# Kernel tuning notes

Hardware: AMD Instinct MI355X
Metric: run time of the kernel (lower is better)

## Reference

```python
import jax, jax.numpy as jnp
import numpy as np

LN_EPS = 1e-5

def _layer_norm(x, w, b):
    mu = jnp.mean(x, axis=-1, keepdims=True)
    var = jnp.mean(jnp.square(x - mu), axis=-1, keepdims=True)
    return (x - mu) * jax.lax.rsqrt(var + LN_EPS) * w + b

def setup_inputs() -> dict:
    key = jax.random.key(0)
    ks = jax.random.split(key, 8)
    B, NODES, D = 32, 202, 64
    return {
        "embeddings": jax.random.normal(ks[0], (B, NODES, D), dtype=jnp.float32),
        "ln_w": jnp.ones((D,), jnp.float32),
        "ln_b": jnp.zeros((D,), jnp.float32),
        "W1_w": jax.random.normal(ks[1], (D, D), jnp.float32) * 0.05,
        "W1_b": jax.random.normal(ks[2], (D,), jnp.float32) * 0.05,
        "W2_w": jax.random.normal(ks[3], (D, D), jnp.float32) * 0.05,
        "W2_b": jax.random.normal(ks[4], (D,), jnp.float32) * 0.05,
        "a1_w": jax.random.normal(ks[5], (3 * D,), jnp.float32) * 0.05,
        "a1_b": jax.random.normal(ks[6], (1,), jnp.float32) * 0.05,
        "a2_w": jax.random.normal(ks[7], (3 * D,), jnp.float32) * 0.05,
        "a2_b": jax.random.normal(jax.random.fold_in(key, 99), (1,), jnp.float32) * 0.05,
    }

def reference(embeddings, ln_w, ln_b, W1_w, W1_b, W2_w, W2_b, a1_w, a1_b, a2_w, a2_b):
    # embeddings: [B, 2+N, D]; dropout p=0 (eval) -> identity
    emb = _layer_norm(embeddings, ln_w, ln_b)
    uid0 = emb[:, 0, :]          # [B, D]
    iid0 = emb[:, 1, :]          # [B, D]
    iatt = emb[:, 2:, :]         # [B, N, D]
    ua = uid0[:, None, :] * iatt  # [B, N, D]
    # value[b,i,j,:] = LN(ua[b,i] * ua[b,j])  -- the big [B,N,N,D] tensor
    value = _layer_norm(ua[:, :, None, :] * ua[:, None, :, :], ln_w, ln_b)

    def head(Ww, Wb, aw, ab):
        # Linear W applied to expanded query/key/iid collapses to per-row projections;
        # a([wq; wk; wiid]) decomposes additively across the three concat blocks.
        wua = ua @ Ww.T + Wb                  # [B, N, D]  (shared by query rows and key cols)
        wiid = iid0 @ Ww.T + Wb               # [B, D]
        aq, ak, ai = jnp.split(aw, 3)
        sq = wua @ aq                         # [B, N]  query contribution (index i)
        sk = wua @ ak                         # [B, N]  key contribution (index j)
        si = wiid @ ai                        # [B]
        scores = sq[:, :, None] + sk[:, None, :] + si[:, None, None] + ab[0]  # [B,N,N]
        scores = jax.nn.leaky_relu(scores)    # negative_slope=0.01 (torch default)
        alphas = jax.nn.softmax(scores, axis=-1)
        # original sums over dim=-2 (index i), softmax was over j -- kept faithfully
        return jnp.einsum('bij,bijd->bjd', alphas, value)  # [B, N, D]

    att1 = head(W1_w, W1_b, a1_w, a1_b)
    att2 = head(W2_w, W2_b, a2_w, a2_b)
    att_value = (att1 + att2) * 0.5           # [B, N, D]
    ui = (uid0 * iid0)[:, None, :]            # [B, 1, D]
    em_out = jnp.concatenate([ui, att_value], axis=1)  # [B, N+1, D]
    return jax.nn.leaky_relu(em_out)
```

## Files before the change

kernel.cpp:

```cpp
#include <hip/hip_runtime.h>
#include <hip/hip_bf16.h>

#define LN_EPS 1e-5f
#define BB 32
#define NI 200
#define DD 64

typedef __attribute__((ext_vector_type(8))) short bf16x8;
typedef __attribute__((ext_vector_type(4))) short bf16x4;
typedef __attribute__((ext_vector_type(4))) float f32x4;

__device__ __forceinline__ float leaky(float x) { return fmaxf(x, 0.01f * x); }
__device__ __forceinline__ short f2bf(float x) {
  __hip_bfloat16 h = __float2bfloat16(x);
  return *reinterpret_cast<short*>(&h);
}
__device__ __forceinline__ float bf2fs(short s) {
  unsigned u = ((unsigned)(unsigned short)s) << 16;
  return __uint_as_float(u);
}

__device__ __forceinline__ void reduce2(float& a, float& b) {
#pragma unroll
  for (int m = 1; m < 64; m <<= 1) { a += __shfl_xor(a, m, 64); b += __shfl_xor(b, m, 64); }
}
__device__ __forceinline__ void reduce3(float& a, float& b, float& c) {
#pragma unroll
  for (int m = 1; m < 64; m <<= 1) {
    a += __shfl_xor(a, m, 64); b += __shfl_xor(b, m, 64); c += __shfl_xor(c, m, 64);
  }
}
__device__ __forceinline__ void rmax2(float& a, float& b) {
#pragma unroll
  for (int m = 1; m < 64; m <<= 1) {
    a = fmaxf(a, __shfl_xor(a, m, 64));
    b = fmaxf(b, __shfl_xor(b, m, 64));
  }
}

#define SM_G    0
#define SM_UA   52544
#define SM_UA2  79168
#define SM_UAT  105792
#define SM_ST   134464
#define SM_KV   139456
#define SM_V    141120
#define SM_PART 142656
#define SM_WMX  143680
#define SM_MISC 143744
#define SM_LN   143776
#define SM_TOTAL 145408

__global__ void __launch_bounds__(512, 1)
gat_fused(const float* __restrict__ emb,
          const float* __restrict__ lw,
          const float* __restrict__ lb,
          const float* __restrict__ W1,
          const float* __restrict__ W1b,
          const float* __restrict__ W2,
          const float* __restrict__ W2b,
          const float* __restrict__ a1,
          const float* __restrict__ a1b,
          const float* __restrict__ a2,
          const float* __restrict__ a2b,
          float* __restrict__ out) {
  __shared__ __align__(16) char smem[SM_TOTAL];
  float* sY   = (float*)(smem + SM_G);
  short* sUA  = (short*)(smem + SM_UA);
  short* sUA2 = (short*)(smem + SM_UA2);
  short* sUAT = (short*)(smem + SM_UAT);
  float* sST  = (float*)(smem + SM_ST);
  float* sKV  = (float*)(smem + SM_KV);
  float* sV   = (float*)(smem + SM_V);
  float* sPart = (float*)(smem + SM_PART);
  float* wmx  = (float*)(smem + SM_WMX);
  float* sMisc = (float*)(smem + SM_MISC);
  float* sLN  = (float*)(smem + SM_LN);

  int b = blockIdx.y, bx = blockIdx.x, tid = threadIdx.x;
  int wv = tid >> 6, lane = tid & 63, q = lane >> 4, col = lane & 15;

  for (int idx = tid; idx < 202 * 16; idx += 512) {
    int r = idx >> 4, qd = (idx & 15) << 2;
    f32x4 v = *(const f32x4*)(emb + ((size_t)b * 202 + r) * 64 + qd);
    float* dst = sY + r * 65 + qd;
    dst[0] = v.x; dst[1] = v.y; dst[2] = v.z; dst[3] = v.w;
  }
  if (wv == 0) {
    float p0 = 0, p1 = 0;
#pragma unroll 8
    for (int d = 0; d < 64; d++) {
      float x = W1[d * 64 + lane];
      p0 = fmaf(x, a1[d], p0); p1 = fmaf(x, a1[64 + d], p1);
    }
    sV[0 * 64 + lane] = p0; sV[1 * 64 + lane] = p1;
  } else if (wv == 1) {
    float p0 = 0, p1 = 0;
#pragma unroll 8
    for (int d = 0; d < 64; d++) {
      float x = W2[d * 64 + lane];
      p0 = fmaf(x, a2[d], p0); p1 = fmaf(x, a2[64 + d], p1);
    }
    sV[2 * 64 + lane] = p0; sV[3 * 64 + lane] = p1;
  } else if (wv == 2) {
    float p = 0;
#pragma unroll 8
    for (int d = 0; d < 64; d++) p = fmaf(W1[d * 64 + lane], a1[128 + d], p);
    sV[4 * 64 + lane] = p;
    float c0 = W1b[lane] * a1[lane];
    float c1 = W1b[lane] * a1[64 + lane];
    float c2 = W1b[lane] * a1[128 + lane];
    reduce3(c0, c1, c2);
    if (lane == 0) { sMisc[0] = c0; sMisc[1] = c1; sMisc[2] = c2; }
  } else if (wv == 3) {
    float p = 0;
#pragma unroll 8
    for (int d = 0; d < 64; d++) p = fmaf(W2[d * 64 + lane], a2[128 + d], p);
    sV[5 * 64 + lane] = p;
    float c3 = W2b[lane] * a2[lane];
    float c4 = W2b[lane] * a2[64 + lane];
    float c5 = W2b[lane] * a2[128 + lane];
    reduce3(c3, c4, c5);
    if (lane == 0) { sMisc[3] = c3; sMisc[4] = c4; sMisc[5] = c5; }
  }
  __syncthreads();

  {
    int o = tid & 7, rr = tid >> 3;
#pragma unroll
    for (int r0 = 0; r0 < 256; r0 += 64) {
      int r = r0 + rr;
      float s = 0.f, s2 = 0.f;
      if (r < 202) {
        const float* xr = sY + r * 65 + o * 8;
#pragma unroll
        for (int k = 0; k < 8; k++) { float x = xr[k]; s += x; s2 = fmaf(x, x, s2); }
      }
#pragma unroll
      for (int m = 1; m < 8; m <<= 1) {
        s += __shfl_xor(s, m, 64); s2 += __shfl_xor(s2, m, 64);
      }
      if (r < 202 && o == 0) {
        float mu = s * (1.f / 64);
        float var = fmaxf(s2 * (1.f / 64) - mu * mu, 0.f);
        sLN[r * 2] = mu;
        sLN[r * 2 + 1] = rsqrtf(var + LN_EPS);
      }
    }
  }
  __syncthreads();

  {
    int d = tid & 63;
    float w = lw[d], bi = lb[d];
    for (int idx = tid; idx < 202 * 64; idx += 512) {
      int r = idx >> 6;
      float mu = sLN[r * 2], rinv = sLN[r * 2 + 1];
      float x = sY[r * 65 + d];
      sY[r * 65 + d] = (x - mu) * rinv * w + bi;
    }
  }
  __syncthreads();

  if (wv == 0) {
    float u0 = sY[lane];
    float iid = sY[65 + lane];
    out[(size_t)(b * 201) * 64 + lane] = leaky(u0 * iid);
    float q0 = iid * sV[4 * 64 + lane], q1 = iid * sV[5 * 64 + lane];
    reduce2(q0, q1);
    if (lane == 0) {
      sMisc[6] = q0 + sMisc[2] + a1b[0];
      sMisc[7] = q1 + sMisc[5] + a2b[0];
    }
  }
  for (int idx = tid; idx < 1664; idx += 512) {
    int itile = idx >> 7, rem = idx & 127, kh = rem >> 6, ln = rem & 63;
    int node = itile * 16 + (ln & 15);
    int dbase = kh * 32 + (ln >> 4) * 8;
    bf16x8 pk, pk2;
    if (node < NI) {
      const float* yr = sY + (2 + node) * 65 + dbase;
#pragma unroll
      for (int k = 0; k < 8; k++) {
        float v = sY[dbase + k] * yr[k];
        short h = f2bf(v);
        pk[k] = h;
        float f = bf2fs(h);
        pk2[k] = f2bf(f * f);
      }
    } else {
#pragma unroll
      for (int k = 0; k < 8; k++) { pk[k] = 0; pk2[k] = 0; }
    }
    *(bf16x8*)(sUA + idx * 8) = pk;
    *(bf16x8*)(sUA2 + idx * 8) = pk2;
  }
  {
    int d = tid & 63, ir = (tid >> 6) & 3, ph = tid >> 8;
    float ud = sY[d];
    for (int p = ph; p < 7; p += 2) {
      int i0 = p * 32 + ir * 8;
      bf16x8 pk;
#pragma unroll
      for (int uu = 0; uu < 8; uu++) {
        int node = i0 + uu;
        pk[uu] = (node < NI) ? f2bf(ud * sY[(2 + node) * 65 + d]) : (short)0;
      }
      int off = ((p * 4 + (d >> 4)) * 64 + ((d & 15) + 16 * ir)) * 8;
      *(bf16x8*)(sUAT + off) = pk;
    }
  }
  {
    int o = tid & 7, rr = tid >> 3;
    float uv0[8], uv1[8], uv2[8], uv3[8];
#pragma unroll
    for (int k = 0; k < 8; k++) {
      float u0k = sY[o * 8 + k];
      uv0[k] = u0k * sV[0 * 64 + o * 8 + k];
      uv1[k] = u0k * sV[1 * 64 + o * 8 + k];
      uv2[k] = u0k * sV[2 * 64 + o * 8 + k];
      uv3[k] = u0k * sV[3 * 64 + o * 8 + k];
    }
#pragma unroll
    for (int r0 = 0; r0 < 256; r0 += 64) {
      int i = r0 + rr;
      float p0 = 0, p1 = 0, p2 = 0, p3 = 0;
      if (i < NI) {
        const float* yr = sY + (2 + i) * 65 + o * 8;
#pragma unroll
        for (int k = 0; k < 8; k++) {
          float y = yr[k];
          p0 = fmaf(y, uv0[k], p0); p1 = fmaf(y, uv1[k], p1);
          p2 = fmaf(y, uv2[k], p2); p3 = fmaf(y, uv3[k], p3);
        }
      }
#pragma unroll
      for (int m = 1; m < 8; m <<= 1) {
        p0 += __shfl_xor(p0, m, 64); p1 += __shfl_xor(p1, m, 64);
        p2 += __shfl_xor(p2, m, 64); p3 += __shfl_xor(p3, m, 64);
      }
      if (i < NI && o == 0) {
        sST[i * 6 + 0] = p0 + sMisc[0];
        sST[i * 6 + 3] = p2 + sMisc[3];
        sKV[0 * 208 + i] = p1 + sMisc[1];
        sKV[1 * 208 + i] = p3 + sMisc[4];
      }
    }
  }
  if (tid < 48) sST[1200 + tid] = 0.f;
  if (tid < 16) sKV[(tid >> 3) * 208 + 200 + (tid & 7)] = 0.f;
  __syncthreads();

  {
    float m1 = (tid < NI) ? sKV[tid] : -3e38f;
    float m2 = (tid < NI) ? sKV[208 + tid] : -3e38f;
    rmax2(m1, m2);
    if (lane == 0) { wmx[wv * 2] = m1; wmx[wv * 2 + 1] = m2; }
  }
  __syncthreads();

  {
    int sh = -1, si = 0;
    if (tid < NI) { sh = 0; si = tid; }
    else if (tid >= 256 && tid < 256 + NI) { sh = 1; si = tid - 256; }
    if (sh >= 0) {
      float mx = -3e38f;
#pragma unroll
      for (int k = 0; k < 8; k++) mx = fmaxf(mx, wmx[k * 2 + sh]);
      float* st = sST + si * 6;
      float base = st[sh * 3] + sMisc[6 + sh];
      st[sh * 3] = base;
      float rm = leaky(base + mx);
      const float* skh = sKV + sh * 208;
      float d0 = 0, d1 = 0, d2 = 0, d3 = 0;
      for (int j = 0; j < NI; j += 4) {
        float s0 = base + skh[j + 0]; d0 += __expf(fmaxf(s0, 0.01f * s0) - rm);
        float s1 = base + skh[j + 1]; d1 += __expf(fmaxf(s1, 0.01f * s1) - rm);
        float s2 = base + skh[j + 2]; d2 += __expf(fmaxf(s2, 0.01f * s2) - rm);
        float s3 = base + skh[j + 3]; d3 += __expf(fmaxf(s3, 0.01f * s3) - rm);
      }
      st[sh * 3 + 1] = rm;
      st[sh * 3 + 2] = 1.0f / ((d0 + d1) + (d2 + d3));
    }
  }
  __syncthreads();

  int half = wv >> 2, wq = wv & 3;
  int jt = bx * 2 + half;
  bool act = (jt < 13);
  short* sG0 = (short*)(smem + SM_G);
  short* sG1 = (short*)(smem + SM_G + 7168);
  short* sGh = half ? sG1 : sG0;
  float* sPh = sPart + half * 128;

  if (tid < 128) ((int*)sG0)[1664 + tid] = 0;
  else if (tid < 256) ((int*)sG1)[1664 + (tid - 128)] = 0;

  if (act) {
    bf16x8 bf0 = *(bf16x8*)(sUA + ((jt * 2 + 0) * 64 + lane) * 8);
    bf16x8 bf1 = *(bf16x8*)(sUA + ((jt * 2 + 1) * 64 + lane) * 8);
    bf16x8 b2f0 = *(bf16x8*)(sUA2 + ((jt * 2 + 0) * 64 + lane) * 8);
    bf16x8 b2f1 = *(bf16x8*)(sUA2 + ((jt * 2 + 1) * 64 + lane) * 8);
    int jglob = jt * 16 + col;
    float skj1 = sKV[jglob], skj2 = sKV[208 + jglob];
    float mpart = 0.f, spart = 0.f;
    for (int it = wq; it < 13; it += 4) {
      bf16x8 af0 = *(bf16x8*)(sUA + ((it * 2 + 0) * 64 + lane) * 8);
      bf16x8 af1 = *(bf16x8*)(sUA + ((it * 2 + 1) * 64 + lane) * 8);
      bf16x8 a2f0 = *(bf16x8*)(sUA2 + ((it * 2 + 0) * 64 + lane) * 8);
      bf16x8 a2f1 = *(bf16x8*)(sUA2 + ((it * 2 + 1) * 64 + lane) * 8);
      f32x4 s = {0, 0, 0, 0}, t = {0, 0, 0, 0};
      s = __builtin_amdgcn_mfma_f32_16x16x32_bf16(af0, bf0, s, 0, 0, 0);
      s = __builtin_amdgcn_mfma_f32_16x16x32_bf16(af1, bf1, s, 0, 0, 0);
      t = __builtin_amdgcn_mfma_f32_16x16x32_bf16(a2f0, b2f0, t, 0, 0, 0);
      t = __builtin_amdgcn_mfma_f32_16x16x32_bf16(a2f1, b2f1, t, 0, 0, 0);
      bf16x4 gp;
#pragma unroll
      for (int r = 0; r < 4; r++) {
        int i = it * 16 + q * 4 + r;
        const float* st = sST + i * 6;
        float mu = s[r] * (1.f / 64);
        float var = fmaxf(t[r] * (1.f / 64) - mu * mu, 0.f);
        float inv = rsqrtf(var + LN_EPS);
        float sc1 = st[0] + skj1;
        float e1 = __expf(fmaxf(sc1, 0.01f * sc1) - st[1]) * st[2];
        float sc2 = st[3] + skj2;
        float e2 = __expf(fmaxf(sc2, 0.01f * sc2) - st[4]) * st[5];
        float c = 0.5f * (e1 + e2);
        float g = c * inv;
        mpart = fmaf(g, mu, mpart);
        spart += c;
        gp[r] = f2bf(g);
      }
      int kl = (it & 1) * 16 + q * 4;
      int off = ((it >> 1) * 64 + (col + 16 * (kl >> 3))) * 8 + (kl & 7);
      *(bf16x4*)(sGh + off) = gp;
    }
    mpart += __shfl_xor(mpart, 16, 64); mpart += __shfl_xor(mpart, 32, 64);
    spart += __shfl_xor(spart, 16, 64); spart += __shfl_xor(spart, 32, 64);
    if (lane < 16) {
      sPh[(wq * 2 + 0) * 16 + lane] = mpart;
      sPh[(wq * 2 + 1) * 16 + lane] = spart;
    }
  }
  __syncthreads();

  if (act) {
    f32x4 acc = {0, 0, 0, 0};
#pragma unroll
    for (int kt = 0; kt < 7; kt++) {
      bf16x8 ga = *(bf16x8*)(sGh + (kt * 64 + lane) * 8);
      bf16x8 ub = *(bf16x8*)(sUAT + ((kt * 4 + wq) * 64 + lane) * 8);
      acc = __builtin_amdgcn_mfma_f32_16x16x32_bf16(ga, ub, acc, 0, 0, 0);
    }
    int d = wq * 16 + col;
    float w = lw[d], bia = lb[d];
#pragma unroll
    for (int r = 0; r < 4; r++) {
      int jl = q * 4 + r, jg = jt * 16 + jl;
      if (jg < NI) {
        float m = sPh[0 * 16 + jl] + sPh[2 * 16 + jl] +
                  sPh[4 * 16 + jl] + sPh[6 * 16 + jl];
        float S = sPh[1 * 16 + jl] + sPh[3 * 16 + jl] +
                  sPh[5 * 16 + jl] + sPh[7 * 16 + jl];
        int cn = jt * 128 + (d >> 5) * 64 + ((d >> 3) & 3) * 16 + (jg & 15);
        float uajd = bf2fs(sUA[cn * 8 + (d & 7)]);
        float att = w * (uajd * acc[r] - m) + bia * S;
        out[(size_t)(b * 201 + 1 + jg) * 64 + d] = leaky(att);
      }
    }
  }
}

extern "C" void kernel_launch(void* const* d_in, const int* in_sizes, int n_in,
                              void* d_out, int out_size, void* d_ws, size_t ws_size,
                              hipStream_t stream) {
  const float* emb = (const float*)d_in[0];
  const float* lw  = (const float*)d_in[1];
  const float* lb  = (const float*)d_in[2];
  const float* W1  = (const float*)d_in[3];
  const float* W1b = (const float*)d_in[4];
  const float* W2  = (const float*)d_in[5];
  const float* W2b = (const float*)d_in[6];
  const float* a1  = (const float*)d_in[7];
  const float* a1b = (const float*)d_in[8];
  const float* a2  = (const float*)d_in[9];
  const float* a2b = (const float*)d_in[10];
  float* out = (float*)d_out;

  gat_fused<<<dim3(7, BB), dim3(512), 0, stream>>>(emb, lw, lb, W1, W1b, W2, W2b,
                                                   a1, a1b, a2, a2b, out);
}
```

Baseline: 94.48 us.

## Split fused kernel into three stages to deduplicate per-batch preprocessing

Before this change, each of the 7 blocks per batch redundantly recomputed LayerNorm, the bf16 ua/ua² tiles, the transposed tiles, the projections and the softmax statistics. Now a first kernel spreads that preprocessing over 13 node tiles per batch and writes it to workspace. A second kernel computes the row max and softmax denominators, and the main kernel only copies the staged data from global memory into shared memory. This removes redundant work and adds parallelism to the prologue, at the cost of two extra launches and a global-memory round trip.

New measurement: 93.90 us. About the same (-0.6%).

```diff
diff --git a/kernel.cpp b/kernel.cpp
--- a/kernel.cpp
+++ b/kernel.cpp
@@ -38,52 +38,49 @@
   }
 }
 
-#define SM_G    0
-#define SM_UA   52544
-#define SM_UA2  79168
-#define SM_UAT  105792
-#define SM_ST   134464
-#define SM_KV   139456
-#define SM_V    141120
-#define SM_PART 142656
-#define SM_WMX  143680
-#define SM_MISC 143744
-#define SM_LN   143776
-#define SM_TOTAL 145408
-
-__global__ void __launch_bounds__(512, 1)
-gat_fused(const float* __restrict__ emb,
-          const float* __restrict__ lw,
-          const float* __restrict__ lb,
-          const float* __restrict__ W1,
-          const float* __restrict__ W1b,
-          const float* __restrict__ W2,
-          const float* __restrict__ W2b,
-          const float* __restrict__ a1,
-          const float* __restrict__ a1b,
-          const float* __restrict__ a2,
-          const float* __restrict__ a2b,
-          float* __restrict__ out) {
-  __shared__ __align__(16) char smem[SM_TOTAL];
-  float* sY   = (float*)(smem + SM_G);
-  short* sUA  = (short*)(smem + SM_UA);
-  short* sUA2 = (short*)(smem + SM_UA2);
-  short* sUAT = (short*)(smem + SM_UAT);
-  float* sST  = (float*)(smem + SM_ST);
-  float* sKV  = (float*)(smem + SM_KV);
-  float* sV   = (float*)(smem + SM_V);
-  float* sPart = (float*)(smem + SM_PART);
-  float* wmx  = (float*)(smem + SM_WMX);
-  float* sMisc = (float*)(smem + SM_MISC);
-  float* sLN  = (float*)(smem + SM_LN);
-
-  int b = blockIdx.y, bx = blockIdx.x, tid = threadIdx.x;
-  int wv = tid >> 6, lane = tid & 63, q = lane >> 4, col = lane & 15;
-
-  for (int idx = tid; idx < 202 * 16; idx += 512) {
+#define WB_STRIDE 88576
+#define WB_UA2    26624
+#define WB_UAT    53248
+#define WB_ST     81920
+#define WB_KV     86912
+#define WX_RAWD   2834432
+#define WX_TD     2940928
+#define WX_CR     2941184
+
+__global__ void __launch_bounds__(256)
+gat_k1(const float* __restrict__ emb,
+       const float* __restrict__ lw,
+       const float* __restrict__ lb,
+       const float* __restrict__ W1,
+       const float* __restrict__ W1b,
+       const float* __restrict__ W2,
+       const float* __restrict__ W2b,
+       const float* __restrict__ a1,
+       const float* __restrict__ a2,
+       float* __restrict__ ws,
+       float* __restrict__ out) {
+  __shared__ float sE[18 * 65];
+  __shared__ float sV[4 * 64];
+  __shared__ float sVi[2 * 64];
+  __shared__ float sLN[18 * 2];
+
+  int b = blockIdx.y, it = blockIdx.x, tid = threadIdx.x;
+  int wv = tid >> 6, lane = tid & 63;
+
+  char* wsb = (char*)ws + (size_t)b * WB_STRIDE;
+  short* wUA  = (short*)wsb;
+  short* wUA2 = (short*)(wsb + WB_UA2);
+  short* wUAT = (short*)(wsb + WB_UAT);
+  float* wRAW = (float*)((char*)ws + WX_RAWD) + (size_t)b * 832;
+  float* wTD  = (float*)((char*)ws + WX_TD) + b * 2;
+  float* wCR  = (float*)((char*)ws + WX_CR) + b * 6;
+
+  for (int idx = tid; idx < 288; idx += 256) {
     int r = idx >> 4, qd = (idx & 15) << 2;
-    f32x4 v = *(const f32x4*)(emb + ((size_t)b * 202 + r) * 64 + qd);
-    float* dst = sY + r * 65 + qd;
+    int g = (r < 2) ? r : 2 + it * 16 + (r - 2);
+    f32x4 v = {0, 0, 0, 0};
+    if (g <= 201) v = *(const f32x4*)(emb + ((size_t)b * 202 + g) * 64 + qd);
+    float* dst = sE + r * 65 + qd;
     dst[0] = v.x; dst[1] = v.y; dst[2] = v.z; dst[3] = v.w;
   }
   if (wv == 0) {
@@ -102,50 +99,46 @@
       p0 = fmaf(x, a2[d], p0); p1 = fmaf(x, a2[64 + d], p1);
     }
     sV[2 * 64 + lane] = p0; sV[3 * 64 + lane] = p1;
-  } else if (wv == 2) {
+  } else if (wv == 2 && it == 0) {
     float p = 0;
 #pragma unroll 8
     for (int d = 0; d < 64; d++) p = fmaf(W1[d * 64 + lane], a1[128 + d], p);
-    sV[4 * 64 + lane] = p;
+    sVi[lane] = p;
     float c0 = W1b[lane] * a1[lane];
     float c1 = W1b[lane] * a1[64 + lane];
     float c2 = W1b[lane] * a1[128 + lane];
     reduce3(c0, c1, c2);
-    if (lane == 0) { sMisc[0] = c0; sMisc[1] = c1; sMisc[2] = c2; }
-  } else if (wv == 3) {
+    if (lane == 0) { wCR[0] = c0; wCR[1] = c1; wCR[2] = c2; }
+  } else if (wv == 3 && it == 0) {
     float p = 0;
 #pragma unroll 8
     for (int d = 0; d < 64; d++) p = fmaf(W2[d * 64 + lane], a2[128 + d], p);
-    sV[5 * 64 + lane] = p;
+    sVi[64 + lane] = p;
     float c3 = W2b[lane] * a2[lane];
     float c4 = W2b[lane] * a2[64 + lane];
     float c5 = W2b[lane] * a2[128 + lane];
     reduce3(c3, c4, c5);
-    if (lane == 0) { sMisc[3] = c3; sMisc[4] = c4; sMisc[5] = c5; }
+    if (lane == 0) { wCR[3] = c3; wCR[4] = c4; wCR[5] = c5; }
   }
   __syncthreads();
 
   {
     int o = tid & 7, rr = tid >> 3;
-#pragma unroll
-    for (int r0 = 0; r0 < 256; r0 += 64) {
-      int r = r0 + rr;
-      float s = 0.f, s2 = 0.f;
-      if (r < 202) {
-        const float* xr = sY + r * 65 + o * 8;
-#pragma unroll
-        for (int k = 0; k < 8; k++) { float x = xr[k]; s += x; s2 = fmaf(x, x, s2); }
-      }
-#pragma unroll
-      for (int m = 1; m < 8; m <<= 1) {
-        s += __shfl_xor(s, m, 64); s2 += __shfl_xor(s2, m, 64);
-      }
-      if (r < 202 && o == 0) {
-        float mu = s * (1.f / 64);
-        float var = fmaxf(s2 * (1.f / 64) - mu * mu, 0.f);
-        sLN[r * 2] = mu;
-        sLN[r * 2 + 1] = rsqrtf(var + LN_EPS);
-      }
+    float s = 0.f, s2 = 0.f;
+    if (rr < 18) {
+      const float* xr = sE + rr * 65 + o * 8;
+#pragma unroll
+      for (int k = 0; k < 8; k++) { float x = xr[k]; s += x; s2 = fmaf(x, x, s2); }
+    }
+#pragma unroll
+    for (int m = 1; m < 8; m <<= 1) {
+      s += __shfl_xor(s, m, 64); s2 += __shfl_xor(s2, m, 64);
+    }
+    if (rr < 18 && o == 0) {
+      float mu = s * (1.f / 64);
+      float var = fmaxf(s2 * (1.f / 64) - mu * mu, 0.f);
+      sLN[rr * 2] = mu;
+      sLN[rr * 2 + 1] = rsqrtf(var + LN_EPS);
     }
   }
   __syncthreads();
@@ -153,36 +146,32 @@
   {
     int d = tid & 63;
     float w = lw[d], bi = lb[d];
-    for (int idx = tid; idx < 202 * 64; idx += 512) {
+    for (int idx = tid; idx < 18 * 64; idx += 256) {
       int r = idx >> 6;
       float mu = sLN[r * 2], rinv = sLN[r * 2 + 1];
-      float x = sY[r * 65 + d];
-      sY[r * 65 + d] = (x - mu) * rinv * w + bi;
-    }
-  }
-  __syncthreads();
-
-  if (wv == 0) {
-    float u0 = sY[lane];
-    float iid = sY[65 + lane];
+      float x = sE[r * 65 + d];
+      sE[r * 65 + d] = (x - mu) * rinv * w + bi;
+    }
+  }
+  __syncthreads();
+
+  if (it == 0 && wv == 2) {
+    float u0 = sE[lane], iid = sE[65 + lane];
     out[(size_t)(b * 201) * 64 + lane] = leaky(u0 * iid);
-    float q0 = iid * sV[4 * 64 + lane], q1 = iid * sV[5 * 64 + lane];
+    float q0 = iid * sVi[lane], q1 = iid * sVi[64 + lane];
     reduce2(q0, q1);
-    if (lane == 0) {
-      sMisc[6] = q0 + sMisc[2] + a1b[0];
-      sMisc[7] = q1 + sMisc[5] + a2b[0];
-    }
-  }
-  for (int idx = tid; idx < 1664; idx += 512) {
-    int itile = idx >> 7, rem = idx & 127, kh = rem >> 6, ln = rem & 63;
-    int node = itile * 16 + (ln & 15);
-    int dbase = kh * 32 + (ln >> 4) * 8;
+    if (lane == 0) { wTD[0] = q0; wTD[1] = q1; }
+  }
+  if (tid < 128) {
+    int rem = tid, kh = rem >> 6, ln = rem & 63;
+    int lnode = ln & 15, g = it * 16 + lnode;
+    int dbase = kh * 32 + (ln >> 4) * 8, lr = 2 + lnode;
     bf16x8 pk, pk2;
-    if (node < NI) {
-      const float* yr = sY + (2 + node) * 65 + dbase;
+    if (g < NI) {
+      const float* yr = sE + lr * 65 + dbase;
 #pragma unroll
       for (int k = 0; k < 8; k++) {
-        float v = sY[dbase + k] * yr[k];
+        float v = sE[dbase + k] * yr[k];
         short h = f2bf(v);
         pk[k] = h;
         float f = bf2fs(h);
@@ -192,109 +181,177 @@
 #pragma unroll
       for (int k = 0; k < 8; k++) { pk[k] = 0; pk2[k] = 0; }
     }
-    *(bf16x8*)(sUA + idx * 8) = pk;
-    *(bf16x8*)(sUA2 + idx * 8) = pk2;
-  }
-  {
-    int d = tid & 63, ir = (tid >> 6) & 3, ph = tid >> 8;
-    float ud = sY[d];
-    for (int p = ph; p < 7; p += 2) {
-      int i0 = p * 32 + ir * 8;
-      bf16x8 pk;
-#pragma unroll
-      for (int uu = 0; uu < 8; uu++) {
-        int node = i0 + uu;
-        pk[uu] = (node < NI) ? f2bf(ud * sY[(2 + node) * 65 + d]) : (short)0;
-      }
-      int off = ((p * 4 + (d >> 4)) * 64 + ((d & 15) + 16 * ir)) * 8;
-      *(bf16x8*)(sUAT + off) = pk;
-    }
-  }
-  {
+    *(bf16x8*)(wUA + (it * 128 + rem) * 8) = pk;
+    *(bf16x8*)(wUA2 + (it * 128 + rem) * 8) = pk2;
+  } else {
+    int tid2 = tid - 128, d = tid2 & 63;
+    int ir = (it & 1) * 2 + (tid2 >> 6), p = it >> 1;
+    int i0 = p * 32 + ir * 8, ln0 = i0 - it * 16;
+    float ud = sE[d];
+    bf16x8 pk;
+#pragma unroll
+    for (int uu = 0; uu < 8; uu++) {
+      int node = i0 + uu;
+      pk[uu] = (node < NI) ? f2bf(ud * sE[(2 + ln0 + uu) * 65 + d]) : (short)0;
+    }
+    int off = ((p * 4 + (d >> 4)) * 64 + ((d & 15) + 16 * ir)) * 8;
+    *(bf16x8*)(wUAT + off) = pk;
+    if (it == 12) {
+      bf16x8 z;
+#pragma unroll
+      for (int uu = 0; uu < 8; uu++) z[uu] = 0;
+      int off2 = ((p * 4 + (d >> 4)) * 64 + ((d & 15) + 16 * (ir + 2))) * 8;
+      *(bf16x8*)(wUAT + off2) = z;
+    }
+  }
+  if (tid < 128) {
     int o = tid & 7, rr = tid >> 3;
-    float uv0[8], uv1[8], uv2[8], uv3[8];
-#pragma unroll
-    for (int k = 0; k < 8; k++) {
-      float u0k = sY[o * 8 + k];
-      uv0[k] = u0k * sV[0 * 64 + o * 8 + k];
-      uv1[k] = u0k * sV[1 * 64 + o * 8 + k];
-      uv2[k] = u0k * sV[2 * 64 + o * 8 + k];
-      uv3[k] = u0k * sV[3 * 64 + o * 8 + k];
-    }
-#pragma unroll
-    for (int r0 = 0; r0 < 256; r0 += 64) {
-      int i = r0 + rr;
+    int i = it * 16 + rr;
+    if (i < NI) {
+      float uv0[8], uv1[8], uv2[8], uv3[8];
+#pragma unroll
+      for (int k = 0; k < 8; k++) {
+        float u0k = sE[o * 8 + k];
+        uv0[k] = u0k * sV[0 * 64 + o * 8 + k];
+        uv1[k] = u0k * sV[1 * 64 + o * 8 + k];
+        uv2[k] = u0k * sV[2 * 64 + o * 8 + k];
+        uv3[k] = u0k * sV[3 * 64 + o * 8 + k];
+      }
+      const float* yr = sE + (2 + rr) * 65 + o * 8;
       float p0 = 0, p1 = 0, p2 = 0, p3 = 0;
-      if (i < NI) {
-        const float* yr = sY + (2 + i) * 65 + o * 8;
-#pragma unroll
-        for (int k = 0; k < 8; k++) {
-          float y = yr[k];
-          p0 = fmaf(y, uv0[k], p0); p1 = fmaf(y, uv1[k], p1);
-          p2 = fmaf(y, uv2[k], p2); p3 = fmaf(y, uv3[k], p3);
-        }
+#pragma unroll
+      for (int k = 0; k < 8; k++) {
+        float y = yr[k];
+        p0 = fmaf(y, uv0[k], p0); p1 = fmaf(y, uv1[k], p1);
+        p2 = fmaf(y, uv2[k], p2); p3 = fmaf(y, uv3[k], p3);
       }
 #pragma unroll
       for (int m = 1; m < 8; m <<= 1) {
         p0 += __shfl_xor(p0, m, 64); p1 += __shfl_xor(p1, m, 64);
         p2 += __shfl_xor(p2, m, 64); p3 += __shfl_xor(p3, m, 64);
       }
-      if (i < NI && o == 0) {
-        sST[i * 6 + 0] = p0 + sMisc[0];
-        sST[i * 6 + 3] = p2 + sMisc[3];
-        sKV[0 * 208 + i] = p1 + sMisc[1];
-        sKV[1 * 208 + i] = p3 + sMisc[4];
-      }
-    }
-  }
-  if (tid < 48) sST[1200 + tid] = 0.f;
-  if (tid < 16) sKV[(tid >> 3) * 208 + 200 + (tid & 7)] = 0.f;
+      if (o == 0) {
+        wRAW[i * 4 + 0] = p0; wRAW[i * 4 + 1] = p1;
+        wRAW[i * 4 + 2] = p2; wRAW[i * 4 + 3] = p3;
+      }
+    }
+  }
+}
+
+__global__ void __launch_bounds__(512)
+gat_k2(float* __restrict__ ws,
+       const float* __restrict__ a1b,
+       const float* __restrict__ a2b) {
+  __shared__ float skv[2 * 208];
+  __shared__ float wmx[16];
+  int b = blockIdx.y, bx = blockIdx.x, tid = threadIdx.x;
+  int wv = tid >> 6, lane = tid & 63;
+
+  char* wsb = (char*)ws + (size_t)b * WB_STRIDE;
+  float* wST = (float*)(wsb + WB_ST);
+  float* wKV = (float*)(wsb + WB_KV);
+  const float* wRAW = (const float*)((char*)ws + WX_RAWD) + (size_t)b * 832;
+  const float* wTD  = (const float*)((char*)ws + WX_TD) + b * 2;
+  const float* wCR  = (const float*)((char*)ws + WX_CR) + b * 6;
+
+  float c0 = wCR[0], c1 = wCR[1], c2 = wCR[2];
+  float c3 = wCR[3], c4 = wCR[4], c5 = wCR[5];
+  float t1 = (wTD[0] + c2) + a1b[0];
+  float t2 = (wTD[1] + c5) + a2b[0];
+
+  if (tid < 208) {
+    float s1 = 0.f, s2 = 0.f;
+    if (tid < NI) {
+      s1 = wRAW[tid * 4 + 1] + c1;
+      s2 = wRAW[tid * 4 + 3] + c4;
+    }
+    skv[tid] = s1; skv[208 + tid] = s2;
+    if (bx == 0) { wKV[tid] = s1; wKV[208 + tid] = s2; }
+  }
   __syncthreads();
 
   {
-    float m1 = (tid < NI) ? sKV[tid] : -3e38f;
-    float m2 = (tid < NI) ? sKV[208 + tid] : -3e38f;
+    float m1 = (tid < NI) ? skv[tid] : -3e38f;
+    float m2 = (tid < NI) ? skv[208 + tid] : -3e38f;
     rmax2(m1, m2);
     if (lane == 0) { wmx[wv * 2] = m1; wmx[wv * 2 + 1] = m2; }
   }
   __syncthreads();
 
   {
-    int sh = -1, si = 0;
-    if (tid < NI) { sh = 0; si = tid; }
-    else if (tid >= 256 && tid < 256 + NI) { sh = 1; si = tid - 256; }
-    if (sh >= 0) {
-      float mx = -3e38f;
-#pragma unroll
-      for (int k = 0; k < 8; k++) mx = fmaxf(mx, wmx[k * 2 + sh]);
-      float* st = sST + si * 6;
-      float base = st[sh * 3] + sMisc[6 + sh];
-      st[sh * 3] = base;
-      float rm = leaky(base + mx);
-      const float* skh = sKV + sh * 208;
-      float d0 = 0, d1 = 0, d2 = 0, d3 = 0;
-      for (int j = 0; j < NI; j += 4) {
-        float s0 = base + skh[j + 0]; d0 += __expf(fmaxf(s0, 0.01f * s0) - rm);
-        float s1 = base + skh[j + 1]; d1 += __expf(fmaxf(s1, 0.01f * s1) - rm);
-        float s2 = base + skh[j + 2]; d2 += __expf(fmaxf(s2, 0.01f * s2) - rm);
-        float s3 = base + skh[j + 3]; d3 += __expf(fmaxf(s3, 0.01f * s3) - rm);
-      }
-      st[sh * 3 + 1] = rm;
-      st[sh * 3 + 2] = 1.0f / ((d0 + d1) + (d2 + d3));
-    }
-  }
+    int o = tid & 3, item = tid >> 2;
+    int rl = item >> 1, sh = item & 1;
+    if (rl < 52) {
+      int r = bx * 52 + rl;
+      if (r < 208) {
+        float* st = wST + r * 6 + sh * 3;
+        if (r < NI) {
+          float mx = -3e38f;
+#pragma unroll
+          for (int k = 0; k < 8; k++) mx = fmaxf(mx, wmx[k * 2 + sh]);
+          float base = (wRAW[r * 4 + (sh ? 2 : 0)] + (sh ? c3 : c0)) + (sh ? t2 : t1);
+          float rm = leaky(base + mx);
+          const float* skh = skv + sh * 208;
+          float den = 0.f;
+          int j0 = o * 50;
+#pragma unroll 5
+          for (int j = j0; j < j0 + 50; j++) {
+            float s = base + skh[j];
+            den += __expf(fmaxf(s, 0.01f * s) - rm);
+          }
+          den += __shfl_xor(den, 1, 64);
+          den += __shfl_xor(den, 2, 64);
+          if (o == 0) { st[0] = base; st[1] = rm; st[2] = 1.0f / den; }
+        } else if (o == 0) {
+          st[0] = 0.f; st[1] = 0.f; st[2] = 0.f;
+        }
+      }
+    }
+  }
+}
+
+#define L_G1    7168
+#define L_STAGE 14336
+#define L_UA    14336
+#define L_UA2   40960
+#define L_UAT   67584
+#define L_ST    96256
+#define L_KV    101248
+#define L_PART  102912
+#define L_TOTAL 103936
+
+__global__ void __launch_bounds__(512, 1)
+gat_k3(const float* __restrict__ ws,
+       const float* __restrict__ lw,
+       const float* __restrict__ lb,
+       float* __restrict__ out) {
+  __shared__ __align__(16) char smem[L_TOTAL];
+  short* sUA  = (short*)(smem + L_UA);
+  short* sUA2 = (short*)(smem + L_UA2);
+  short* sUAT = (short*)(smem + L_UAT);
+  float* sST  = (float*)(smem + L_ST);
+  float* sKV  = (float*)(smem + L_KV);
+  float* sPart = (float*)(smem + L_PART);
+
+  int b = blockIdx.y, bx = blockIdx.x, tid = threadIdx.x;
+  int wv = tid >> 6, lane = tid & 63, q = lane >> 4, col = lane & 15;
+
+  {
+    const f32x4* src = (const f32x4*)((const char*)ws + (size_t)b * WB_STRIDE);
+    f32x4* dst = (f32x4*)(smem + L_STAGE);
+    for (int idx = tid; idx < WB_STRIDE / 16; idx += 512) dst[idx] = src[idx];
+  }
+  short* sG0 = (short*)smem;
+  short* sG1 = (short*)(smem + L_G1);
+  if (tid < 128) ((int*)sG0)[1664 + tid] = 0;
+  else if (tid < 256) ((int*)sG1)[1664 + (tid - 128)] = 0;
   __syncthreads();
 
   int half = wv >> 2, wq = wv & 3;
   int jt = bx * 2 + half;
   bool act = (jt < 13);
-  short* sG0 = (short*)(smem + SM_G);
-  short* sG1 = (short*)(smem + SM_G + 7168);
   short* sGh = half ? sG1 : sG0;
   float* sPh = sPart + half * 128;
-
-  if (tid < 128) ((int*)sG0)[1664 + tid] = 0;
-  else if (tid < 256) ((int*)sG1)[1664 + (tid - 128)] = 0;
 
   if (act) {
     bf16x8 bf0 = *(bf16x8*)(sUA + ((jt * 2 + 0) * 64 + lane) * 8);
@@ -386,8 +443,11 @@
   const float* a1b = (const float*)d_in[8];
   const float* a2  = (const float*)d_in[9];
   const float* a2b = (const float*)d_in[10];
+  float* ws = (float*)d_ws;
   float* out = (float*)d_out;
 
-  gat_fused<<<dim3(7, BB), dim3(512), 0, stream>>>(emb, lw, lb, W1, W1b, W2, W2b,
-                                                   a1, a1b, a2, a2b, out);
-}
+  gat_k1<<<dim3(13, BB), dim3(256), 0, stream>>>(emb, lw, lb, W1, W1b, W2, W2b,
+                                                 a1, a2, ws, out);
+  gat_k2<<<dim3(4, BB), dim3(512), 0, stream>>>(ws, a1b, a2b);
+  gat_k3<<<dim3(7, BB), dim3(512), 0, stream>>>(ws, lw, lb, out);
+}
```
